# Performance work log

Measured on AMD Instinct MI355X. Metric: run time of the kernel, lower is better.

## Reference

```python
import jax, jax.numpy as jnp
import numpy as np

N, E, G = 10000, 100000, 16
NS, NV = 128, 64            # scalar (0e) / vector (1o) channel counts
DIM = NS + 3 * NV           # 320 flattened feature dim
NSP = 4                     # num_species; edge one-hot has NSP**2 entries
FC_IN = 128                 # edge length embedding size
GATES = NV                  # one gate scalar per gated vector channel
EPS = 1e-5


def _split(x):
    # flattened irreps layout: [NS scalars | NV vectors * 3 components]
    return x[:, :NS], x[:, NS:].reshape(x.shape[0], NV, 3)


def _merge(s, v):
    return jnp.concatenate([s, v.reshape(v.shape[0], -1)], axis=-1)


def setup_inputs() -> dict:
    key = jax.random.key(0)
    ks = jax.random.split(key, 32)
    def nrm(i, shape):
        return jax.random.normal(ks[i], shape, jnp.float32)
    return {
        'node_fea': nrm(0, (N, DIM)),
        'edge_one_hot': jax.random.uniform(ks[1], (E, NSP * NSP), jnp.float32),
        'edge_sh': nrm(2, (E, 4)),
        'edge_fea': nrm(3, (E, DIM)),
        'edge_length_embedded': jax.random.uniform(ks[4], (E, FC_IN), jnp.float32),
        'edge_index': jax.random.randint(ks[5], (2, E), 0, N),
        'batch': jnp.sort(jax.random.randint(ks[6], (N,), 0, G)),
        # self-connection FCTP: edge irreps x species-pair scalars -> out irreps
        'Wsc_s': nrm(7, (NS, NSP * NSP, NS)),
        'Wsc_v': nrm(8, (NV, NSP * NSP, NV)),
        # lin_pre (per-l equivariant linear, bias on scalars only)
        'Wpre0': nrm(9, (NS, NS)), 'bpre0': jnp.zeros((NS,), jnp.float32),
        'Wpre1': nrm(10, (NV, NV)),
        # separate-weight tensor product paths (fea_in x spherical harmonics)
        'Wss': nrm(11, (3 * NS, NS + GATES)),   # 0e x 0e -> 0e
        'Wvs': nrm(12, (3 * NV, NS + GATES)),   # 1o . 1o -> 0e
        'Wsv': nrm(13, (3 * NS, NV)),           # 0e x 1o -> 1o
        'Wvv': nrm(14, (3 * NV, NV)),           # 1o x 0e -> 1o
        # radial MLP (fc): edge_length_embedded -> per-channel conv weights
        'Wf1': nrm(15, (FC_IN, 64)) / np.sqrt(FC_IN), 'bf1': jnp.zeros((64,), jnp.float32),
        'Wf2': nrm(16, (64, 64)) / 8.0, 'bf2': jnp.zeros((64,), jnp.float32),
        'Wf3': nrm(17, (64, NS + NV)) / 8.0, 'bf3': jnp.zeros((NS + NV,), jnp.float32),
        # lin_post
        'Wpost0': nrm(18, (NS, NS)), 'bpost0': jnp.zeros((NS,), jnp.float32),
        'Wpost1': nrm(19, (NV, NV)),
        # e3LayerNorm affine params
        'gamma_s': jnp.ones((NS,), jnp.float32), 'beta_s': jnp.zeros((NS,), jnp.float32),
        'gamma_v': jnp.ones((NV,), jnp.float32),
    }


def reference(node_fea, edge_one_hot, edge_sh, edge_fea, edge_length_embedded,
              edge_index, batch, Wsc_s, Wsc_v, Wpre0, bpre0, Wpre1,
              Wss, Wvs, Wsv, Wvv, Wf1, bf1, Wf2, bf2, Wf3, bf3,
              Wpost0, bpost0, Wpost1, gamma_s, beta_s, gamma_v):
    i, j = edge_index[0], edge_index[1]
    batch_edge = batch[i]
    es, ev = _split(edge_fea)

    # --- self connection: FullyConnectedTensorProduct(edge_fea, one_hot) ---
    sc_s = jnp.einsum('ev,es,vsu->eu', es, edge_one_hot, Wsc_s) / np.sqrt(NS * NSP * NSP)
    sc_v = jnp.einsum('evm,es,vsu->eum', ev, edge_one_hot, Wsc_v) / np.sqrt(NV * NSP * NSP)

    # --- lin_pre on edge features ---
    s = es @ Wpre0 / np.sqrt(NS) + bpre0
    v = jnp.einsum('evm,vu->eum', ev, Wpre1) / np.sqrt(NV)

    # --- gather node features and concat along channel axis ---
    nsf, nvf = _split(node_fea)
    s_in = jnp.concatenate([nsf[i], nsf[j], s], axis=-1)   # [E, 3*NS]
    v_in = jnp.concatenate([nvf[i], nvf[j], v], axis=1)    # [E, 3*NV, 3]

    sh0, sh1 = edge_sh[:, :1], edge_sh[:, 1:4]
    # --- separate-weight tensor product (CG: 1o x 1o -> 0e via dot/sqrt(3)) ---
    out_s = (jnp.einsum('ev,vu->eu', s_in * sh0, Wss) / np.sqrt(3 * NS)
             + jnp.einsum('evm,em,vu->eu', v_in, sh1, Wvs) / np.sqrt(3 * 3 * NV)) / np.sqrt(2.0)
    out_v = (jnp.einsum('ev,em,vu->eum', s_in, sh1, Wsv) / np.sqrt(3 * NS)
             + jnp.einsum('evm,e,vu->eum', v_in, sh0[:, 0], Wvv) / np.sqrt(3 * NV)) / np.sqrt(2.0)

    # --- gate nonlinearity: silu on scalars, sigmoid gates on vectors ---
    z_s = jax.nn.silu(out_s[:, :NS])
    z_v = out_v * jax.nn.sigmoid(out_s[:, NS:])[:, :, None]

    # --- radial MLP -> e3ElementWise per-channel scaling ---
    h = jax.nn.silu(edge_length_embedded @ Wf1 + bf1)
    h = jax.nn.silu(h @ Wf2 + bf2)
    w = h @ Wf3 + bf3                                      # [E, NS+NV]
    z_s = z_s * w[:, :NS]
    z_v = z_v * w[:, NS:, None]

    # --- lin_post ---
    z_s = z_s @ Wpost0 / np.sqrt(NS) + bpost0
    z_v = jnp.einsum('evm,vu->eum', z_v, Wpost1) / np.sqrt(NV)

    # --- add self connection ---
    z_s = z_s + sc_s
    z_v = z_v + sc_v

    # --- e3LayerNorm with per-graph statistics over edges ---
    cnt = jax.ops.segment_sum(jnp.ones((E,), z_s.dtype), batch_edge, num_segments=G)
    cnt = jnp.maximum(cnt, 1.0)
    mean_s = jax.ops.segment_sum(z_s.sum(-1), batch_edge, num_segments=G) / (cnt * NS)
    z_s = z_s - mean_s[batch_edge][:, None]
    var_s = jax.ops.segment_sum((z_s ** 2).sum(-1), batch_edge, num_segments=G) / (cnt * NS)
    z_s = z_s * jax.lax.rsqrt(var_s + EPS)[batch_edge][:, None] * gamma_s + beta_s
    var_v = jax.ops.segment_sum((z_v ** 2).sum((-1, -2)), batch_edge, num_segments=G) / (cnt * NV * 3)
    z_v = z_v * jax.lax.rsqrt(var_v + EPS)[batch_edge][:, None, None] * gamma_v[None, :, None]

    # --- skip connection (same irreps in/out -> plain add) ---
    return edge_fea + _merge(z_s, z_v)
```

## Files before the change

### kernel.cpp

```cpp
#include <hip/hip_runtime.h>
#include <math.h>

typedef unsigned int u32;
typedef unsigned short u16;
typedef __attribute__((ext_vector_type(8))) short bf16x8;
typedef __attribute__((ext_vector_type(4))) float f32x4;

#define E_TOT 100000
constexpr int NS = 128, DIM = 320;

constexpr float SC_S_SCALE = 0.022097086912079608f;
constexpr float SC_V_SCALE = 0.03125f;
constexpr float INV_SQRT128 = 0.08838834764831845f;
constexpr float INV_8 = 0.125f;
constexpr float INV_S384 = 0.05103103630798288f;
constexpr float INV_24 = 0.041666666666666664f;
constexpr float INV_S192 = 0.07216878364870323f;
constexpr float RSQRT2 = 0.7071067811865476f;

#define MFMA __builtin_amdgcn_mfma_f32_16x16x32_bf16
#define F4Z (f32x4){0.f, 0.f, 0.f, 0.f}

__device__ __forceinline__ float sigmoidf_(float x) { return 1.0f / (1.0f + __expf(-x)); }
__device__ __forceinline__ float siluf_(float x) { return x * sigmoidf_(x); }
__device__ __forceinline__ float bf2f(u16 h) {
  u32 u = ((u32)h) << 16;
  return __builtin_bit_cast(float, u);
}
__device__ __forceinline__ u16 f2bf(float f) {
  u32 u = __builtin_bit_cast(u32, f);
  return (u16)((u + 0x7fffu + ((u >> 16) & 1u)) >> 16);
}
__device__ __forceinline__ void gl_lds16(const void* g, void* l) {
  __builtin_amdgcn_global_load_lds((const __attribute__((address_space(1))) u32*)g,
                                   (__attribute__((address_space(3))) u32*)l, 16, 0, 0);
}
__device__ __forceinline__ bf16x8 pack8(float4 r0, float4 r1, float s) {
  bf16x8 a;
  a[0] = (short)f2bf(r0.x * s); a[1] = (short)f2bf(r0.y * s);
  a[2] = (short)f2bf(r0.z * s); a[3] = (short)f2bf(r0.w * s);
  a[4] = (short)f2bf(r1.x * s); a[5] = (short)f2bf(r1.y * s);
  a[6] = (short)f2bf(r1.z * s); a[7] = (short)f2bf(r1.w * s);
  return a;
}
__device__ __forceinline__ void stb(char* base, int row, int rowB, int colByte, u16 v) {
  *(u16*)(base + row * rowB + (colByte ^ ((row & 7) << 4))) = v;
}
__device__ __forceinline__ u16 ldbs(const char* base, int row, int rowB, int colByte) {
  return *(const u16*)(base + row * rowB + (colByte ^ ((row & 7) << 4)));
}
__device__ __forceinline__ bf16x8 ldb8(const char* base, int row, int rowB, int colByte) {
  return *(const bf16x8*)(base + row * rowB + (colByte ^ ((row & 7) << 4)));
}
__device__ __forceinline__ void stb16(char* base, int row, int rowB, int colByte, bf16x8 v) {
  *(bf16x8*)(base + row * rowB + (colByte ^ ((row & 7) << 4))) = v;
}
__device__ __forceinline__ bf16x8 scale8_sh1(bf16x8 v, int m0, float t0, float t1, float t2) {
  float x0 = (m0 == 0) ? t0 : ((m0 == 1) ? t1 : t2);
  float x1 = (m0 == 0) ? t1 : ((m0 == 1) ? t2 : t0);
  float x2 = (m0 == 0) ? t2 : ((m0 == 1) ? t0 : t1);
  bf16x8 r;
  r[0] = (short)f2bf(bf2f((u16)v[0]) * x0); r[1] = (short)f2bf(bf2f((u16)v[1]) * x1);
  r[2] = (short)f2bf(bf2f((u16)v[2]) * x2); r[3] = (short)f2bf(bf2f((u16)v[3]) * x0);
  r[4] = (short)f2bf(bf2f((u16)v[4]) * x1); r[5] = (short)f2bf(bf2f((u16)v[5]) * x2);
  r[6] = (short)f2bf(bf2f((u16)v[6]) * x0); r[7] = (short)f2bf(bf2f((u16)v[7]) * x1);
  return r;
}

#define OW_W2S   0
#define OW_BTV   262144
#define OW_PRE0  327680
#define OW_PRE1X 344064
#define OW_SS    380928
#define OW_VSX   454656
#define OW_SV    565248
#define OW_VVX   589824
#define OW_F1    700416
#define OW_F2    708608
#define OW_F3    712704
#define OW_P0    724992
#define OW_P1X   741376
#define OW_END   778240

__device__ __forceinline__ void frag_uc(int oo, int K, int& up, int& c) {
  int per = (K >> 5) << 9;
  int nt = oo / per, r = oo % per;
  int kc = r >> 9, r2 = r & 511;
  int ln = r2 >> 3, j = r2 & 7;
  up = nt * 16 + (ln & 15);
  c = kc * 32 + (ln >> 4) * 8 + j;
}

__global__ __launch_bounds__(256) void k_prep(
    const float* __restrict__ Wsc_s, const float* __restrict__ Wsc_v,
    const float* __restrict__ Wpre0, const float* __restrict__ Wpre1,
    const float* __restrict__ Wss, const float* __restrict__ Wvs,
    const float* __restrict__ Wsv, const float* __restrict__ Wvv,
    const float* __restrict__ Wf1, const float* __restrict__ Wf2,
    const float* __restrict__ Wf3, const float* __restrict__ Wpost0,
    const float* __restrict__ Wpost1, u16* __restrict__ dst) {
  int o = blockIdx.x * 256 + threadIdx.x;
  if (o >= OW_END) return;
  float v;
  int up, c;
  if (o < OW_BTV) {
    int u = o >> 11, k = o & 2047, s = k >> 7, vv = k & 127;
    v = Wsc_s[((size_t)(vv * 16 + s)) * 128 + u];
  } else if (o < OW_PRE0) {
    int oo = o - OW_BTV; int u = oo >> 10, k = oo & 1023, s = k >> 6, vv = k & 63;
    v = Wsc_v[((size_t)(vv * 16 + s)) * 64 + u];
  } else if (o < OW_PRE1X) {
    frag_uc(o - OW_PRE0, 128, up, c);
    v = Wpre0[c * 128 + up] * INV_SQRT128;
  } else if (o < OW_SS) {
    frag_uc(o - OW_PRE1X, 192, up, c);
    int u = up / 3, m = up % 3, vv = c / 3, mp = c % 3;
    v = (m == mp) ? Wpre1[vv * 64 + u] * INV_8 : 0.f;
  } else if (o < OW_VSX) {
    frag_uc(o - OW_SS, 384, up, c);
    v = Wss[c * 192 + up] * (INV_S384 * RSQRT2);
  } else if (o < OW_SV) {
    frag_uc(o - OW_VSX, 576, up, c);
    int p = c / 192, r = c % 192, K = p * 64 + r / 3;
    v = Wvs[K * 192 + up] * (INV_24 * RSQRT2);
  } else if (o < OW_VVX) {
    frag_uc(o - OW_SV, 384, up, c);
    v = Wsv[c * 64 + up] * (INV_S384 * RSQRT2);
  } else if (o < OW_F1) {
    frag_uc(o - OW_VVX, 576, up, c);
    int u = up / 3, m = up % 3, p = c / 192, r = c % 192, vv = r / 3, mp = r % 3;
    v = (m == mp) ? Wvv[(p * 64 + vv) * 64 + u] * (INV_S192 * RSQRT2) : 0.f;
  } else if (o < OW_F2) {
    frag_uc(o - OW_F1, 128, up, c);
    v = Wf1[c * 64 + up];
  } else if (o < OW_F3) {
    frag_uc(o - OW_F2, 64, up, c);
    v = Wf2[c * 64 + up];
  } else if (o < OW_P0) {
    frag_uc(o - OW_F3, 64, up, c);
    v = Wf3[c * 192 + up];
  } else if (o < OW_P1X) {
    frag_uc(o - OW_P0, 128, up, c);
    v = Wpost0[c * 128 + up] * INV_SQRT128;
  } else {
    frag_uc(o - OW_P1X, 192, up, c);
    int u = up / 3, m = up % 3, vv = c / 3, mp = c % 3;
    v = (m == mp) ? Wpost1[vv * 64 + u] * INV_8 : 0.f;
  }
  dst[o] = f2bf(v);
}

#define MEs 64
__global__ __launch_bounds__(256, 2) void k_sc_s(
    const float* __restrict__ edge_fea, const float* __restrict__ ohp,
    const u16* __restrict__ W2s, float* __restrict__ out) {
  __shared__ u16 esB[64][136];
  __shared__ float ohL[64][16];
  __shared__ u16 Abuf[64 * 128];
  __shared__ u16 Bbuf[128 * 128];
  const int t = threadIdx.x;
  const int lane = t & 63, ww = t >> 6;
  const int e0 = blockIdx.x * MEs;
  const int nE = min(MEs, E_TOT - e0);

  for (int o = t; o < 64 * 32; o += 256) {
    int e = o >> 5, c4 = (o & 31) << 2;
    float4 x = (e < nE) ? *(const float4*)&edge_fea[(size_t)(e0 + e) * DIM + c4]
                        : make_float4(0.f, 0.f, 0.f, 0.f);
    esB[e][c4 + 0] = f2bf(x.x); esB[e][c4 + 1] = f2bf(x.y);
    esB[e][c4 + 2] = f2bf(x.z); esB[e][c4 + 3] = f2bf(x.w);
  }
  for (int o = t; o < 64 * 16; o += 256) {
    int e = o >> 4, s = o & 15;
    ohL[e][s] = (e < nE) ? ohp[(size_t)(e0 + e) * 16 + s] : 0.f;
  }
  __syncthreads();

  f32x4 acc[4][2];
  #pragma unroll
  for (int a = 0; a < 4; ++a)
    #pragma unroll
    for (int b = 0; b < 2; ++b) acc[a][b] = F4Z;

  for (int s = 0; s < 16; ++s) {
    {
      const char* sb = (const char*)W2s + s * 256;
      #pragma unroll
      for (int it = 0; it < 8; ++it) {
        int n = it * 256 + t;
        int u = n >> 4, gp = n & 15, g = gp ^ (u & 7);
        gl_lds16(sb + (size_t)u * 4096 + g * 16, (char*)Bbuf + n * 16);
      }
    }
    #pragma unroll
    for (int it = 0; it < 4; ++it) {
      int n = it * 256 + t;
      int e = n >> 4, gp = n & 15, g = gp ^ (e & 7);
      float ohs = ohL[e][s];
      union { uint4 q; u16 h[8]; } in, ov;
      in.q = *(const uint4*)&esB[e][g * 8];
      #pragma unroll
      for (int j = 0; j < 8; ++j) ov.h[j] = f2bf(bf2f(in.h[j]) * ohs);
      *(uint4*)((char*)Abuf + e * 256 + gp * 16) = ov.q;
    }
    __syncthreads();

    const int cbl = (lane >> 4) << 4;
    #pragma unroll
    for (int ks = 0; ks < 4; ++ks) {
      int cbyte = ks * 64 + cbl;
      bf16x8 bfr[2], afr[4];
      #pragma unroll
      for (int ct = 0; ct < 2; ++ct) {
        int u = ww * 32 + ct * 16 + (lane & 15);
        bfr[ct] = *(const bf16x8*)((const char*)Bbuf + u * 256 + (cbyte ^ ((u & 7) << 4)));
      }
      #pragma unroll
      for (int rt = 0; rt < 4; ++rt) {
        int e = rt * 16 + (lane & 15);
        afr[rt] = *(const bf16x8*)((const char*)Abuf + e * 256 + (cbyte ^ ((e & 7) << 4)));
      }
      #pragma unroll
      for (int rt = 0; rt < 4; ++rt)
        #pragma unroll
        for (int ct = 0; ct < 2; ++ct)
          acc[rt][ct] = MFMA(afr[rt], bfr[ct], acc[rt][ct], 0, 0, 0);
    }
    __syncthreads();
  }

  #pragma unroll
  for (int rt = 0; rt < 4; ++rt) {
    int ebase = rt * 16 + ((lane >> 4) << 2);
    #pragma unroll
    for (int ct = 0; ct < 2; ++ct) {
      int u = ww * 32 + ct * 16 + (lane & 15);
      #pragma unroll
      for (int j = 0; j < 4; ++j) {
        int ee = ebase + j;
        if (ee < nE) out[(size_t)(e0 + ee) * DIM + u] = acc[rt][ct][j] * SC_S_SCALE;
      }
    }
  }
}

__global__ __launch_bounds__(256, 2) void k_sc_v(
    const float* __restrict__ edge_fea, const float* __restrict__ ohp,
    const u16* __restrict__ Btv, float* __restrict__ out) {
  __shared__ u16 evT[3][64][72];
  __shared__ float ohL[64][16];
  __shared__ u16 Abuf[192 * 64];
  __shared__ u16 Bbuf[64 * 64];
  const int t = threadIdx.x;
  const int lane = t & 63, ww = t >> 6;
  const int e0 = blockIdx.x * MEs;
  const int nE = min(MEs, E_TOT - e0);

  for (int o = t; o < 64 * 192; o += 256) {
    int e = o / 192, c = o % 192;
    int v = c / 3, m = c % 3;
    float x = (e < nE) ? edge_fea[(size_t)(e0 + e) * DIM + NS + c] : 0.f;
    evT[m][e][v] = f2bf(x);
  }
  for (int o = t; o < 64 * 16; o += 256) {
    int e = o >> 4, s = o & 15;
    ohL[e][s] = (e < nE) ? ohp[(size_t)(e0 + e) * 16 + s] : 0.f;
  }
  __syncthreads();

  f32x4 acc[12];
  #pragma unroll
  for (int a = 0; a < 12; ++a) acc[a] = F4Z;

  for (int s = 0; s < 16; ++s) {
    #pragma unroll
    for (int it = 0; it < 2; ++it) {
      int n = it * 256 + t;
      int u = n >> 3, gp = n & 7, g = gp ^ (u & 7);
      gl_lds16((const char*)Btv + (size_t)u * 2048 + s * 128 + g * 16, (char*)Bbuf + n * 16);
    }
    #pragma unroll
    for (int it = 0; it < 6; ++it) {
      int n = it * 256 + t;
      int r = n >> 3, gp = n & 7, g = gp ^ (r & 7);
      int e = r / 3, m = r - e * 3;
      float ohs = ohL[e][s];
      union { uint4 q; u16 h[8]; } in, ov;
      in.q = *(const uint4*)&evT[m][e][g * 8];
      #pragma unroll
      for (int j = 0; j < 8; ++j) ov.h[j] = f2bf(bf2f(in.h[j]) * ohs);
      *(uint4*)((char*)Abuf + r * 128 + gp * 16) = ov.q;
    }
    __syncthreads();

    const int cbl = (lane >> 4) << 4;
    #pragma unroll
    for (int ks = 0; ks < 2; ++ks) {
      int cbyte = ks * 64 + cbl;
      int u = ww * 16 + (lane & 15);
      bf16x8 bfr = *(const bf16x8*)((const char*)Bbuf + u * 128 + (cbyte ^ ((u & 7) << 4)));
      #pragma unroll
      for (int rt = 0; rt < 12; ++rt) {
        int r = rt * 16 + (lane & 15);
        bf16x8 afr = *(const bf16x8*)((const char*)Abuf + r * 128 + (cbyte ^ ((r & 7) << 4)));
        acc[rt] = MFMA(afr, bfr, acc[rt], 0, 0, 0);
      }
    }
    __syncthreads();
  }

  #pragma unroll
  for (int rt = 0; rt < 12; ++rt) {
    int rbase = rt * 16 + ((lane >> 4) << 2);
    int u = ww * 16 + (lane & 15);
    #pragma unroll
    for (int j = 0; j < 4; ++j) {
      int r = rbase + j;
      int e = r / 3, m = r - e * 3;
      if (e < nE) out[(size_t)(e0 + e) * DIM + NS + u * 3 + m] = acc[rt][j] * SC_V_SCALE;
    }
  }
}

#define A_SZ 78592
__global__ __launch_bounds__(512, 4) void k_chain(
    const float* __restrict__ node_fea, const float* __restrict__ edge_sh,
    const float* __restrict__ edge_fea, const float* __restrict__ elen,
    const int* __restrict__ eidx, const u16* __restrict__ wbf,
    const float* __restrict__ bpre0, const float* __restrict__ bf1,
    const float* __restrict__ bf2, const float* __restrict__ bf3,
    const float* __restrict__ bpost0, float* __restrict__ out) {
  __shared__ char AR[A_SZ];
  float* shF = (float*)(AR + 77824);
  int* ijL = (int*)(AR + 78336);
  const int t = threadIdx.x, lane = t & 63, wv = t >> 6;
  const int l15 = lane & 15, q8 = lane >> 4, q4 = q8 << 2, cbl = q8 << 4;
  const int e0 = blockIdx.x * 32;

#define SA(b) (AR + (b) * 8192)
#define VA(b) (AR + 24576 + (b) * 12288)
  char* wB = AR;
  char* zsB = AR + 12288;
  char* gateB = AR + 20480;
  char* zvB = AR + 24576;
  char* t1B = AR + 61440;
  char* hB = AR + 65536;
  char* elB = AR + 69632;

  if (t < 64) { int p = t >> 5, e = t & 31; ijL[p * 32 + e] = eidx[p * E_TOT + e0 + e]; }
  if (t >= 64 && t < 192) { int o = t - 64; shF[o] = edge_sh[(size_t)e0 * 4 + o]; }
  __syncthreads();

  for (int o = t; o < 1280; o += 512) {
    int c = o % 40, e = o / 40;
    const float* src = edge_fea + (size_t)(e0 + e) * 320 + c * 8;
    float4 r0 = *(const float4*)src, r1 = *(const float4*)(src + 4);
    bf16x8 v = pack8(r0, r1, 1.f);
    if (c < 16) stb16(SA(2), e, 256, c * 16, v);
    else        stb16(VA(2), e, 384, (c - 16) * 16, v);
  }
  for (int o = t; o < 2560; o += 512) {
    int c = o % 40, tmp = o / 40, e = tmp & 31, p = tmp >> 5;
    const float* src = node_fea + (size_t)ijL[p * 32 + e] * 320 + c * 8;
    float4 r0 = *(const float4*)src, r1 = *(const float4*)(src + 4);
    bf16x8 v = pack8(r0, r1, 1.f);
    if (c < 16) stb16(SA(p), e, 256, c * 16, v);
    else        stb16(VA(p), e, 384, (c - 16) * 16, v);
  }
  for (int o = t; o < 512; o += 512) {
    int c = o & 15, e = o >> 4;
    const float* src = elen + (size_t)(e0 + e) * 128 + c * 8;
    float4 r0 = *(const float4*)src, r1 = *(const float4*)(src + 4);
    stb16(elB, e, 256, c * 16, pack8(r0, r1, 1.f));
  }
  __syncthreads();

  f32x4 acc[8];
  #pragma unroll
  for (int a = 0; a < 8; ++a) acc[a] = F4Z;
  if (wv < 4) {
    for (int kc = 0; kc < 6; ++kc) {
      bf16x8 a0 = ldb8(VA(2), l15, 384, kc * 64 + cbl);
      bf16x8 a1 = ldb8(VA(2), 16 + l15, 384, kc * 64 + cbl);
      #pragma unroll
      for (int i = 0; i < 3; ++i) {
        int nt = wv * 3 + i;
        bf16x8 b = *(const bf16x8*)(wbf + OW_PRE1X + (((size_t)nt * 6 + kc) << 9) + lane * 8);
        acc[i] = MFMA(a0, b, acc[i], 0, 0, 0);
        acc[3 + i] = MFMA(a1, b, acc[3 + i], 0, 0, 0);
      }
    }
  } else if (wv < 6) {
    for (int kc = 0; kc < 4; ++kc) {
      bf16x8 a0 = ldb8(SA(2), l15, 256, kc * 64 + cbl);
      bf16x8 a1 = ldb8(SA(2), 16 + l15, 256, kc * 64 + cbl);
      #pragma unroll
      for (int i = 0; i < 4; ++i) {
        int nt = (wv - 4) * 4 + i;
        bf16x8 b = *(const bf16x8*)(wbf + OW_PRE0 + (((size_t)nt * 4 + kc) << 9) + lane * 8);
        acc[i] = MFMA(a0, b, acc[i], 0, 0, 0);
        acc[4 + i] = MFMA(a1, b, acc[4 + i], 0, 0, 0);
      }
    }
  } else {
    for (int kc = 0; kc < 4; ++kc) {
      bf16x8 a0 = ldb8(elB, l15, 256, kc * 64 + cbl);
      bf16x8 a1 = ldb8(elB, 16 + l15, 256, kc * 64 + cbl);
      #pragma unroll
      for (int i = 0; i < 2; ++i) {
        int nt = (wv - 6) * 2 + i;
        bf16x8 b = *(const bf16x8*)(wbf + OW_F1 + (((size_t)nt * 4 + kc) << 9) + lane * 8);
        acc[i] = MFMA(a0, b, acc[i], 0, 0, 0);
        acc[2 + i] = MFMA(a1, b, acc[2 + i], 0, 0, 0);
      }
    }
  }
  __syncthreads();
  if (wv < 4) {
    #pragma unroll
    for (int mt = 0; mt < 2; ++mt)
      #pragma unroll
      for (int i = 0; i < 3; ++i) {
        int up = (wv * 3 + i) * 16 + l15;
        #pragma unroll
        for (int j = 0; j < 4; ++j)
          stb(VA(2), mt * 16 + q4 + j, 384, up * 2, f2bf(acc[mt * 3 + i][j]));
      }
  } else if (wv < 6) {
    #pragma unroll
    for (int i = 0; i < 4; ++i) {
      int u = ((wv - 4) * 4 + i) * 16 + l15;
      float bias = bpre0[u];
      #pragma unroll
      for (int mt = 0; mt < 2; ++mt)
        #pragma unroll
        for (int j = 0; j < 4; ++j)
          stb(SA(2), mt * 16 + q4 + j, 256, u * 2, f2bf(acc[mt * 4 + i][j] + bias));
    }
  } else {
    #pragma unroll
    for (int i = 0; i < 2; ++i) {
      int u = ((wv - 6) * 2 + i) * 16 + l15;
      float bias = bf1[u];
      #pragma unroll
      for (int mt = 0; mt < 2; ++mt)
        #pragma unroll
        for (int j = 0; j < 4; ++j)
          stb(hB, mt * 16 + q4 + j, 128, u * 2, f2bf(siluf_(acc[mt * 2 + i][j] + bias)));
    }
  }
  __syncthreads();

  f32x4 os[4] = {F4Z, F4Z, F4Z, F4Z};
  f32x4 h2a = F4Z;
  {
    const int hmt = wv >> 2, hnt = wv & 3;
    #pragma unroll
    for (int kc = 0; kc < 2; ++kc) {
      bf16x8 a = ldb8(hB, hmt * 16 + l15, 128, kc * 64 + cbl);
      bf16x8 b = *(const bf16x8*)(wbf + OW_F2 + (((size_t)hnt * 2 + kc) << 9) + lane * 8);
      h2a = MFMA(a, b, h2a, 0, 0, 0);
    }
  }
  if (wv < 6) {
    for (int kc = 0; kc < 12; ++kc) {
      int buf = kc >> 2, cB = (kc & 3) * 64 + cbl;
      bf16x8 a0 = ldb8(SA(buf), l15, 256, cB);
      bf16x8 a1 = ldb8(SA(buf), 16 + l15, 256, cB);
      #pragma unroll
      for (int i = 0; i < 2; ++i) {
        int nt = wv * 2 + i;
        bf16x8 b = *(const bf16x8*)(wbf + OW_SS + (((size_t)nt * 12 + kc) << 9) + lane * 8);
        os[i] = MFMA(a0, b, os[i], 0, 0, 0);
        os[2 + i] = MFMA(a1, b, os[2 + i], 0, 0, 0);
      }
    }
    #pragma unroll
    for (int mt = 0; mt < 2; ++mt)
      #pragma unroll
      for (int i = 0; i < 2; ++i)
        #pragma unroll
        for (int j = 0; j < 4; ++j)
          os[mt * 2 + i][j] *= shF[(mt * 16 + q4 + j) * 4 + 0];
    float sa0 = shF[l15 * 4 + 1], sa1 = shF[l15 * 4 + 2], sa2 = shF[l15 * 4 + 3];
    float sb0 = shF[(16 + l15) * 4 + 1], sb1 = shF[(16 + l15) * 4 + 2], sb2 = shF[(16 + l15) * 4 + 3];
    for (int p = 0; p < 3; ++p)
      for (int kc6 = 0; kc6 < 6; ++kc6) {
        int cB = kc6 * 64 + cbl;
        int m0 = (2 * (kc6 + q8)) % 3;
        bf16x8 a0 = scale8_sh1(ldb8(VA(p), l15, 384, cB), m0, sa0, sa1, sa2);
        bf16x8 a1 = scale8_sh1(ldb8(VA(p), 16 + l15, 384, cB), m0, sb0, sb1, sb2);
        int kcg = p * 6 + kc6;
        #pragma unroll
        for (int i = 0; i < 2; ++i) {
          int nt = wv * 2 + i;
          bf16x8 b = *(const bf16x8*)(wbf + OW_VSX + (((size_t)nt * 18 + kcg) << 9) + lane * 8);
          os[i] = MFMA(a0, b, os[i], 0, 0, 0);
          os[2 + i] = MFMA(a1, b, os[2 + i], 0, 0, 0);
        }
      }
  } else {
    for (int kc = 0; kc < 12; ++kc) {
      int buf = kc >> 2, cB = (kc & 3) * 64 + cbl;
      bf16x8 a0 = ldb8(SA(buf), l15, 256, cB);
      bf16x8 a1 = ldb8(SA(buf), 16 + l15, 256, cB);
      #pragma unroll
      for (int i = 0; i < 2; ++i) {
        int nt = (wv - 6) * 2 + i;
        bf16x8 b = *(const bf16x8*)(wbf + OW_SV + (((size_t)nt * 12 + kc) << 9) + lane * 8);
        os[i] = MFMA(a0, b, os[i], 0, 0, 0);
        os[2 + i] = MFMA(a1, b, os[2 + i], 0, 0, 0);
      }
    }
  }
  __syncthreads();
  {
    const int hmt = wv >> 2;
    int u = (wv & 3) * 16 + l15;
    float bias = bf2[u];
    #pragma unroll
    for (int j = 0; j < 4; ++j)
      stb(hB, hmt * 16 + q4 + j, 128, u * 2, f2bf(siluf_(h2a[j] + bias)));
  }
  if (wv >= 6) {
    #pragma unroll
    for (int mt = 0; mt < 2; ++mt)
      #pragma unroll
      for (int i = 0; i < 2; ++i) {
        int u = ((wv - 6) * 2 + i) * 16 + l15;
        #pragma unroll
        for (int j = 0; j < 4; ++j)
          stb(t1B, mt * 16 + q4 + j, 128, u * 2, f2bf(os[mt * 2 + i][j]));
      }
  }
  __syncthreads();

  {
    f32x4 wa[3] = {F4Z, F4Z, F4Z};
    const int mtw = wv >> 2;
    #pragma unroll
    for (int kc = 0; kc < 2; ++kc) {
      bf16x8 a = ldb8(hB, mtw * 16 + l15, 128, kc * 64 + cbl);
      #pragma unroll
      for (int i = 0; i < 3; ++i) {
        int nt = (wv & 3) * 3 + i;
        bf16x8 b = *(const bf16x8*)(wbf + OW_F3 + (((size_t)nt * 2 + kc) << 9) + lane * 8);
        wa[i] = MFMA(a, b, wa[i], 0, 0, 0);
      }
    }
    #pragma unroll
    for (int i = 0; i < 3; ++i) {
      int up = ((wv & 3) * 3 + i) * 16 + l15;
      float bias = bf3[up];
      #pragma unroll
      for (int j = 0; j < 4; ++j)
        stb(wB, mtw * 16 + q4 + j, 384, up * 2, f2bf(wa[i][j] + bias));
    }
  }
  __syncthreads();

  if (wv < 6) {
    #pragma unroll
    for (int mt = 0; mt < 2; ++mt)
      #pragma unroll
      for (int i = 0; i < 2; ++i) {
        int up = (wv * 2 + i) * 16 + l15;
        #pragma unroll
        for (int j = 0; j < 4; ++j) {
          int e = mt * 16 + q4 + j;
          float w_ = bf2f(ldbs(wB, e, 384, up * 2));
          float o_ = os[mt * 2 + i][j];
          if (up < 128) stb(zsB, e, 256, up * 2, f2bf(siluf_(o_) * w_));
          else stb(gateB, e, 128, (up - 128) * 2, f2bf(sigmoidf_(o_) * w_));
        }
      }
  }
  f32x4 ov[3] = {F4Z, F4Z, F4Z};
  {
    const int mtv = wv >> 2;
    for (int p = 0; p < 3; ++p)
      for (int kc6 = 0; kc6 < 6; ++kc6) {
        int cB = kc6 * 64 + cbl;
        bf16x8 a = ldb8(VA(p), mtv * 16 + l15, 384, cB);
        int kcg = p * 6 + kc6;
        #pragma unroll
        for (int i = 0; i < 3; ++i) {
          int nt = (wv & 3) * 3 + i;
          bf16x8 b = *(const bf16x8*)(wbf + OW_VVX + (((size_t)nt * 18 + kcg) << 9) + lane * 8);
          ov[i] = MFMA(a, b, ov[i], 0, 0, 0);
        }
      }
  }
  __syncthreads();
  {
    const int mtv = wv >> 2;
    #pragma unroll
    for (int i = 0; i < 3; ++i) {
      int up = ((wv & 3) * 3 + i) * 16 + l15;
      int u = (up * 683) >> 11, m = up - 3 * u;
      #pragma unroll
      for (int j = 0; j < 4; ++j) {
        int e = mtv * 16 + q4 + j;
        float t1v = bf2f(ldbs(t1B, e, 128, u * 2));
        float g = bf2f(ldbs(gateB, e, 128, u * 2));
        float val = ov[i][j] * shF[e * 4 + 0] + t1v * shF[e * 4 + 1 + m];
        stb(zvB, e, 384, up * 2, f2bf(val * g));
      }
    }
  }
  __syncthreads();

  {
    f32x4 p0[2] = {F4Z, F4Z};
    #pragma unroll
    for (int kc = 0; kc < 4; ++kc) {
      int cB = kc * 64 + cbl;
      bf16x8 a0 = ldb8(zsB, l15, 256, cB);
      bf16x8 a1 = ldb8(zsB, 16 + l15, 256, cB);
      bf16x8 b = *(const bf16x8*)(wbf + OW_P0 + (((size_t)wv * 4 + kc) << 9) + lane * 8);
      p0[0] = MFMA(a0, b, p0[0], 0, 0, 0);
      p0[1] = MFMA(a1, b, p0[1], 0, 0, 0);
    }
    int u = wv * 16 + l15;
    float bias = bpost0[u];
    #pragma unroll
    for (int mt = 0; mt < 2; ++mt)
      #pragma unroll
      for (int j = 0; j < 4; ++j) {
        size_t o = (size_t)(e0 + mt * 16 + q4 + j) * DIM + u;
        out[o] = out[o] + p0[mt][j] + bias;
      }
  }
  {
    f32x4 p1[3] = {F4Z, F4Z, F4Z};
    const int mtv = wv >> 2;
    #pragma unroll
    for (int kc = 0; kc < 6; ++kc) {
      int cB = kc * 64 + cbl;
      bf16x8 a = ldb8(zvB, mtv * 16 + l15, 384, cB);
      #pragma unroll
      for (int i = 0; i < 3; ++i) {
        int nt = (wv & 3) * 3 + i;
        bf16x8 b = *(const bf16x8*)(wbf + OW_P1X + (((size_t)nt * 6 + kc) << 9) + lane * 8);
        p1[i] = MFMA(a, b, p1[i], 0, 0, 0);
      }
    }
    #pragma unroll
    for (int i = 0; i < 3; ++i) {
      int up = ((wv & 3) * 3 + i) * 16 + l15;
      #pragma unroll
      for (int j = 0; j < 4; ++j) {
        size_t o = (size_t)(e0 + mtv * 16 + q4 + j) * DIM + 128 + up;
        out[o] = out[o] + p1[i][j];
      }
    }
  }
#undef SA
#undef VA
}

__global__ __launch_bounds__(256) void k_stats(
    const float* __restrict__ out, const int* __restrict__ eidx,
    const int* __restrict__ batch, float* __restrict__ stats) {
  __shared__ float gacc[16][4];
  const int t = threadIdx.x;
  if (t < 64) ((float*)gacc)[t] = 0.0f;
  __syncthreads();
  const int el = t >> 4, l = t & 15;
  for (int ebase = blockIdx.x * 16; ebase < E_TOT; ebase += gridDim.x * 16) {
    int e = ebase + el;
    const float* z = out + (size_t)e * DIM;
    float s1 = 0, s2 = 0, s2v = 0;
    for (int c = l; c < 128; c += 16) { float x = z[c]; s1 += x; s2 += x * x; }
    for (int c = 128 + l; c < DIM; c += 16) { float x = z[c]; s2v += x * x; }
    #pragma unroll
    for (int msk = 8; msk; msk >>= 1) {
      s1 += __shfl_xor(s1, msk);
      s2 += __shfl_xor(s2, msk);
      s2v += __shfl_xor(s2v, msk);
    }
    if (l == 0) {
      int g = batch[eidx[e]];
      atomicAdd(&gacc[g][0], 1.0f);
      atomicAdd(&gacc[g][1], s1);
      atomicAdd(&gacc[g][2], s2);
      atomicAdd(&gacc[g][3], s2v);
    }
  }
  __syncthreads();
  if (t < 64) {
    float v = gacc[t >> 2][t & 3];
    if (v != 0.0f) atomicAdd(&stats[(t >> 2) * 16 + (t & 3)], v);
  }
}

__global__ __launch_bounds__(256) void k_norm(
    const float* __restrict__ edge_fea, const int* __restrict__ eidx,
    const int* __restrict__ batch, const float* __restrict__ stats,
    const float* __restrict__ gamma_s, const float* __restrict__ beta_s,
    const float* __restrict__ gamma_v, float* __restrict__ out) {
  __shared__ float meanL[16], invsL[16], invvL[16];
  __shared__ int gL[16];
  const int t = threadIdx.x;
  const int e0 = blockIdx.x * 16;
  if (t < 16) {
    float cnt = fmaxf(stats[t * 16 + 0], 1.0f);
    float m = stats[t * 16 + 1] / (cnt * 128.0f);
    float var = stats[t * 16 + 2] / (cnt * 128.0f) - m * m;
    meanL[t] = m;
    invsL[t] = rsqrtf(var + 1e-5f);
    invvL[t] = rsqrtf(stats[t * 16 + 3] / (cnt * 192.0f) + 1e-5f);
  }
  if (t >= 32 && t < 48) gL[t - 32] = batch[eidx[e0 + t - 32]];
  __syncthreads();
  for (int o = t; o < 16 * 80; o += 256) {
    int e = o / 80, q = o % 80;
    size_t idx = (size_t)(e0 + e) * 80 + q;
    float4 z = ((const float4*)out)[idx];
    float4 ef = ((const float4*)edge_fea)[idx];
    int g = gL[e];
    float4 r;
    if (q < 32) {
      int c = q * 4;
      r.x = (z.x - meanL[g]) * invsL[g] * gamma_s[c + 0] + beta_s[c + 0] + ef.x;
      r.y = (z.y - meanL[g]) * invsL[g] * gamma_s[c + 1] + beta_s[c + 1] + ef.y;
      r.z = (z.z - meanL[g]) * invsL[g] * gamma_s[c + 2] + beta_s[c + 2] + ef.z;
      r.w = (z.w - meanL[g]) * invsL[g] * gamma_s[c + 3] + beta_s[c + 3] + ef.w;
    } else {
      int cc = q * 4 - 128;
      r.x = z.x * invvL[g] * gamma_v[(cc + 0) / 3] + ef.x;
      r.y = z.y * invvL[g] * gamma_v[(cc + 1) / 3] + ef.y;
      r.z = z.z * invvL[g] * gamma_v[(cc + 2) / 3] + ef.z;
      r.w = z.w * invvL[g] * gamma_v[(cc + 3) / 3] + ef.w;
    }
    ((float4*)out)[idx] = r;
  }
}

extern "C" void kernel_launch(void* const* d_in, const int* in_sizes, int n_in,
                              void* d_out, int out_size, void* d_ws, size_t ws_size,
                              hipStream_t stream) {
  const float* node_fea = (const float*)d_in[0];
  const float* edge_oh  = (const float*)d_in[1];
  const float* edge_sh  = (const float*)d_in[2];
  const float* edge_fea = (const float*)d_in[3];
  const float* elen     = (const float*)d_in[4];
  const int*   eidx     = (const int*)d_in[5];
  const int*   batch    = (const int*)d_in[6];
  const float* Wsc_s    = (const float*)d_in[7];
  const float* Wsc_v    = (const float*)d_in[8];
  const float* Wpre0    = (const float*)d_in[9];
  const float* bpre0    = (const float*)d_in[10];
  const float* Wpre1    = (const float*)d_in[11];
  const float* Wss      = (const float*)d_in[12];
  const float* Wvs      = (const float*)d_in[13];
  const float* Wsv      = (const float*)d_in[14];
  const float* Wvv      = (const float*)d_in[15];
  const float* Wf1      = (const float*)d_in[16];
  const float* bf1      = (const float*)d_in[17];
  const float* Wf2      = (const float*)d_in[18];
  const float* bf2      = (const float*)d_in[19];
  const float* Wf3      = (const float*)d_in[20];
  const float* bf3      = (const float*)d_in[21];
  const float* Wpost0   = (const float*)d_in[22];
  const float* bpost0   = (const float*)d_in[23];
  const float* Wpost1   = (const float*)d_in[24];
  const float* gamma_s  = (const float*)d_in[25];
  const float* beta_s   = (const float*)d_in[26];
  const float* gamma_v  = (const float*)d_in[27];
  float* out = (float*)d_out;

  char* ws = (char*)d_ws;
  float* stats = (float*)ws;
  u16* wbf = (u16*)(ws + 1024);

  hipMemsetAsync(stats, 0, 16 * 16 * sizeof(float), stream);
  k_prep<<<(OW_END + 255) / 256, 256, 0, stream>>>(
      Wsc_s, Wsc_v, Wpre0, Wpre1, Wss, Wvs, Wsv, Wvv,
      Wf1, Wf2, Wf3, Wpost0, Wpost1, wbf);
  const int nblk64 = (E_TOT + MEs - 1) / MEs;
  k_sc_s<<<nblk64, 256, 0, stream>>>(edge_fea, edge_oh, wbf + OW_W2S, out);
  k_sc_v<<<nblk64, 256, 0, stream>>>(edge_fea, edge_oh, wbf + OW_BTV, out);
  k_chain<<<E_TOT / 32, 512, 0, stream>>>(node_fea, edge_sh, edge_fea, elen, eidx,
                                          wbf, bpre0, bf1, bf2, bf3, bpost0, out);
  k_stats<<<512, 256, 0, stream>>>(out, eidx, batch, stats);
  k_norm<<<E_TOT / 16, 256, 0, stream>>>(edge_fea, eidx, batch, stats,
                                         gamma_s, beta_s, gamma_v, out);
}
```

Measured before the change: 760.1 us.

## Fuse self-connection kernels and apply one-hot scaling after MFMA

Merges the scalar and vector self-connection kernels into one launch that reads each edge_fea row once. Instead of rebuilding a one-hot-scaled A tile in LDS for every species pair, it keeps the A fragments fixed (registers for scalars, LDS for vectors), computes the plain product per species pair, and scales the partial result by the one-hot weight in fp32 registers. The output scale constants are folded into the bf16 weights during prep. k_stats is vectorised to use float4 loads. This removes per-iteration A-tile construction and one kernel launch, in exchange for more register pressure and extra fp32 multiply-adds per species pair.

```diff
diff --git a/kernel.cpp b/kernel.cpp
--- a/kernel.cpp
+++ b/kernel.cpp
@@ -105,10 +105,10 @@
   int up, c;
   if (o < OW_BTV) {
     int u = o >> 11, k = o & 2047, s = k >> 7, vv = k & 127;
-    v = Wsc_s[((size_t)(vv * 16 + s)) * 128 + u];
+    v = Wsc_s[((size_t)(vv * 16 + s)) * 128 + u] * SC_S_SCALE;
   } else if (o < OW_PRE0) {
     int oo = o - OW_BTV; int u = oo >> 10, k = oo & 1023, s = k >> 6, vv = k & 63;
-    v = Wsc_v[((size_t)(vv * 16 + s)) * 64 + u];
+    v = Wsc_v[((size_t)(vv * 16 + s)) * 64 + u] * SC_V_SCALE;
   } else if (o < OW_PRE1X) {
     frag_uc(o - OW_PRE0, 128, up, c);
     v = Wpre0[c * 128 + up] * INV_SQRT128;
@@ -151,174 +151,139 @@
 }
 
 #define MEs 64
-__global__ __launch_bounds__(256, 2) void k_sc_s(
+__global__ __launch_bounds__(256, 2) void k_sc(
     const float* __restrict__ edge_fea, const float* __restrict__ ohp,
-    const u16* __restrict__ W2s, float* __restrict__ out) {
-  __shared__ u16 esB[64][136];
+    const u16* __restrict__ W2s, const u16* __restrict__ Btv,
+    float* __restrict__ out) {
+  __shared__ char esB[16384];
+  __shared__ char evT[24576];
   __shared__ float ohL[64][16];
-  __shared__ u16 Abuf[64 * 128];
-  __shared__ u16 Bbuf[128 * 128];
-  const int t = threadIdx.x;
-  const int lane = t & 63, ww = t >> 6;
+  __shared__ char Bbuf[32768];
+  const int t = threadIdx.x, lane = t & 63, ww = t >> 6;
+  const int l15 = lane & 15, q8 = lane >> 4, q4 = q8 << 2, cbl = q8 << 4;
   const int e0 = blockIdx.x * MEs;
   const int nE = min(MEs, E_TOT - e0);
 
-  for (int o = t; o < 64 * 32; o += 256) {
-    int e = o >> 5, c4 = (o & 31) << 2;
-    float4 x = (e < nE) ? *(const float4*)&edge_fea[(size_t)(e0 + e) * DIM + c4]
-                        : make_float4(0.f, 0.f, 0.f, 0.f);
-    esB[e][c4 + 0] = f2bf(x.x); esB[e][c4 + 1] = f2bf(x.y);
-    esB[e][c4 + 2] = f2bf(x.z); esB[e][c4 + 3] = f2bf(x.w);
-  }
-  for (int o = t; o < 64 * 16; o += 256) {
+  for (int o = t; o < 2560; o += 256) {
+    int c = o % 40, e = o / 40;
+    float4 r0 = make_float4(0.f, 0.f, 0.f, 0.f), r1 = r0;
+    if (e < nE) {
+      const float* src = edge_fea + (size_t)(e0 + e) * 320 + c * 8;
+      r0 = *(const float4*)src; r1 = *(const float4*)(src + 4);
+    }
+    if (c < 16) stb16(esB, e, 256, c * 16, pack8(r0, r1, 1.f));
+    else {
+      int base = (c - 16) * 8;
+      float vals[8] = {r0.x, r0.y, r0.z, r0.w, r1.x, r1.y, r1.z, r1.w};
+      #pragma unroll
+      for (int z = 0; z < 8; ++z) {
+        int cc = base + z;
+        stb(evT, 3 * e + cc % 3, 128, (cc / 3) * 2, f2bf(vals[z]));
+      }
+    }
+  }
+  for (int o = t; o < 1024; o += 256) {
     int e = o >> 4, s = o & 15;
     ohL[e][s] = (e < nE) ? ohp[(size_t)(e0 + e) * 16 + s] : 0.f;
   }
   __syncthreads();
 
-  f32x4 acc[4][2];
-  #pragma unroll
-  for (int a = 0; a < 4; ++a)
-    #pragma unroll
-    for (int b = 0; b < 2; ++b) acc[a][b] = F4Z;
-
-  for (int s = 0; s < 16; ++s) {
-    {
+  {
+    bf16x8 afh[4][4];
+    #pragma unroll
+    for (int rt = 0; rt < 4; ++rt)
+      #pragma unroll
+      for (int ks = 0; ks < 4; ++ks)
+        afh[rt][ks] = ldb8(esB, rt * 16 + l15, 256, ks * 64 + cbl);
+    f32x4 acc[8];
+    #pragma unroll
+    for (int i = 0; i < 8; ++i) acc[i] = F4Z;
+    for (int s = 0; s < 16; ++s) {
       const char* sb = (const char*)W2s + s * 256;
       #pragma unroll
       for (int it = 0; it < 8; ++it) {
         int n = it * 256 + t;
         int u = n >> 4, gp = n & 15, g = gp ^ (u & 7);
-        gl_lds16(sb + (size_t)u * 4096 + g * 16, (char*)Bbuf + n * 16);
-      }
-    }
-    #pragma unroll
-    for (int it = 0; it < 4; ++it) {
-      int n = it * 256 + t;
-      int e = n >> 4, gp = n & 15, g = gp ^ (e & 7);
-      float ohs = ohL[e][s];
-      union { uint4 q; u16 h[8]; } in, ov;
-      in.q = *(const uint4*)&esB[e][g * 8];
-      #pragma unroll
-      for (int j = 0; j < 8; ++j) ov.h[j] = f2bf(bf2f(in.h[j]) * ohs);
-      *(uint4*)((char*)Abuf + e * 256 + gp * 16) = ov.q;
-    }
-    __syncthreads();
-
-    const int cbl = (lane >> 4) << 4;
-    #pragma unroll
-    for (int ks = 0; ks < 4; ++ks) {
-      int cbyte = ks * 64 + cbl;
-      bf16x8 bfr[2], afr[4];
+        gl_lds16(sb + (size_t)u * 4096 + g * 16, Bbuf + n * 16);
+      }
+      __syncthreads();
+      f32x4 tmp[8];
+      #pragma unroll
+      for (int i = 0; i < 8; ++i) tmp[i] = F4Z;
+      #pragma unroll
+      for (int ks = 0; ks < 4; ++ks) {
+        bf16x8 b0 = ldb8(Bbuf, ww * 32 + l15, 256, ks * 64 + cbl);
+        bf16x8 b1 = ldb8(Bbuf, ww * 32 + 16 + l15, 256, ks * 64 + cbl);
+        #pragma unroll
+        for (int rt = 0; rt < 4; ++rt) {
+          tmp[rt * 2 + 0] = MFMA(afh[rt][ks], b0, tmp[rt * 2 + 0], 0, 0, 0);
+          tmp[rt * 2 + 1] = MFMA(afh[rt][ks], b1, tmp[rt * 2 + 1], 0, 0, 0);
+        }
+      }
+      #pragma unroll
+      for (int rt = 0; rt < 4; ++rt)
+        #pragma unroll
+        for (int j = 0; j < 4; ++j) {
+          float oh = ohL[rt * 16 + q4 + j][s];
+          acc[rt * 2 + 0][j] += oh * tmp[rt * 2 + 0][j];
+          acc[rt * 2 + 1][j] += oh * tmp[rt * 2 + 1][j];
+        }
+      __syncthreads();
+    }
+    #pragma unroll
+    for (int rt = 0; rt < 4; ++rt)
       #pragma unroll
       for (int ct = 0; ct < 2; ++ct) {
-        int u = ww * 32 + ct * 16 + (lane & 15);
-        bfr[ct] = *(const bf16x8*)((const char*)Bbuf + u * 256 + (cbyte ^ ((u & 7) << 4)));
-      }
-      #pragma unroll
-      for (int rt = 0; rt < 4; ++rt) {
-        int e = rt * 16 + (lane & 15);
-        afr[rt] = *(const bf16x8*)((const char*)Abuf + e * 256 + (cbyte ^ ((e & 7) << 4)));
-      }
-      #pragma unroll
-      for (int rt = 0; rt < 4; ++rt)
-        #pragma unroll
-        for (int ct = 0; ct < 2; ++ct)
-          acc[rt][ct] = MFMA(afr[rt], bfr[ct], acc[rt][ct], 0, 0, 0);
-    }
-    __syncthreads();
-  }
-
-  #pragma unroll
-  for (int rt = 0; rt < 4; ++rt) {
-    int ebase = rt * 16 + ((lane >> 4) << 2);
-    #pragma unroll
-    for (int ct = 0; ct < 2; ++ct) {
-      int u = ww * 32 + ct * 16 + (lane & 15);
+        int u = ww * 32 + ct * 16 + l15;
+        #pragma unroll
+        for (int j = 0; j < 4; ++j) {
+          int e = rt * 16 + q4 + j;
+          if (e < nE) out[(size_t)(e0 + e) * DIM + u] = acc[rt * 2 + ct][j];
+        }
+      }
+  }
+
+  {
+    f32x4 acc[12];
+    #pragma unroll
+    for (int i = 0; i < 12; ++i) acc[i] = F4Z;
+    for (int s = 0; s < 16; ++s) {
+      #pragma unroll
+      for (int it = 0; it < 2; ++it) {
+        int n = it * 256 + t;
+        int u = n >> 3, gp = n & 7, g = gp ^ (u & 7);
+        gl_lds16((const char*)Btv + (size_t)u * 2048 + s * 128 + g * 16, Bbuf + n * 16);
+      }
+      __syncthreads();
+      f32x4 tmp[12];
+      #pragma unroll
+      for (int i = 0; i < 12; ++i) tmp[i] = F4Z;
+      #pragma unroll
+      for (int ks = 0; ks < 2; ++ks) {
+        bf16x8 b = ldb8(Bbuf, ww * 16 + l15, 128, ks * 64 + cbl);
+        #pragma unroll
+        for (int rt = 0; rt < 12; ++rt) {
+          bf16x8 a = ldb8(evT, rt * 16 + l15, 128, ks * 64 + cbl);
+          tmp[rt] = MFMA(a, b, tmp[rt], 0, 0, 0);
+        }
+      }
+      #pragma unroll
+      for (int rt = 0; rt < 12; ++rt)
+        #pragma unroll
+        for (int j = 0; j < 4; ++j) {
+          int r = rt * 16 + q4 + j;
+          acc[rt][j] += ohL[r / 3][s] * tmp[rt][j];
+        }
+      __syncthreads();
+    }
+    int u = ww * 16 + l15;
+    #pragma unroll
+    for (int rt = 0; rt < 12; ++rt)
       #pragma unroll
       for (int j = 0; j < 4; ++j) {
-        int ee = ebase + j;
-        if (ee < nE) out[(size_t)(e0 + ee) * DIM + u] = acc[rt][ct][j] * SC_S_SCALE;
-      }
-    }
-  }
-}
-
-__global__ __launch_bounds__(256, 2) void k_sc_v(
-    const float* __restrict__ edge_fea, const float* __restrict__ ohp,
-    const u16* __restrict__ Btv, float* __restrict__ out) {
-  __shared__ u16 evT[3][64][72];
-  __shared__ float ohL[64][16];
-  __shared__ u16 Abuf[192 * 64];
-  __shared__ u16 Bbuf[64 * 64];
-  const int t = threadIdx.x;
-  const int lane = t & 63, ww = t >> 6;
-  const int e0 = blockIdx.x * MEs;
-  const int nE = min(MEs, E_TOT - e0);
-
-  for (int o = t; o < 64 * 192; o += 256) {
-    int e = o / 192, c = o % 192;
-    int v = c / 3, m = c % 3;
-    float x = (e < nE) ? edge_fea[(size_t)(e0 + e) * DIM + NS + c] : 0.f;
-    evT[m][e][v] = f2bf(x);
-  }
-  for (int o = t; o < 64 * 16; o += 256) {
-    int e = o >> 4, s = o & 15;
-    ohL[e][s] = (e < nE) ? ohp[(size_t)(e0 + e) * 16 + s] : 0.f;
-  }
-  __syncthreads();
-
-  f32x4 acc[12];
-  #pragma unroll
-  for (int a = 0; a < 12; ++a) acc[a] = F4Z;
-
-  for (int s = 0; s < 16; ++s) {
-    #pragma unroll
-    for (int it = 0; it < 2; ++it) {
-      int n = it * 256 + t;
-      int u = n >> 3, gp = n & 7, g = gp ^ (u & 7);
-      gl_lds16((const char*)Btv + (size_t)u * 2048 + s * 128 + g * 16, (char*)Bbuf + n * 16);
-    }
-    #pragma unroll
-    for (int it = 0; it < 6; ++it) {
-      int n = it * 256 + t;
-      int r = n >> 3, gp = n & 7, g = gp ^ (r & 7);
-      int e = r / 3, m = r - e * 3;
-      float ohs = ohL[e][s];
-      union { uint4 q; u16 h[8]; } in, ov;
-      in.q = *(const uint4*)&evT[m][e][g * 8];
-      #pragma unroll
-      for (int j = 0; j < 8; ++j) ov.h[j] = f2bf(bf2f(in.h[j]) * ohs);
-      *(uint4*)((char*)Abuf + r * 128 + gp * 16) = ov.q;
-    }
-    __syncthreads();
-
-    const int cbl = (lane >> 4) << 4;
-    #pragma unroll
-    for (int ks = 0; ks < 2; ++ks) {
-      int cbyte = ks * 64 + cbl;
-      int u = ww * 16 + (lane & 15);
-      bf16x8 bfr = *(const bf16x8*)((const char*)Bbuf + u * 128 + (cbyte ^ ((u & 7) << 4)));
-      #pragma unroll
-      for (int rt = 0; rt < 12; ++rt) {
-        int r = rt * 16 + (lane & 15);
-        bf16x8 afr = *(const bf16x8*)((const char*)Abuf + r * 128 + (cbyte ^ ((r & 7) << 4)));
-        acc[rt] = MFMA(afr, bfr, acc[rt], 0, 0, 0);
-      }
-    }
-    __syncthreads();
-  }
-
-  #pragma unroll
-  for (int rt = 0; rt < 12; ++rt) {
-    int rbase = rt * 16 + ((lane >> 4) << 2);
-    int u = ww * 16 + (lane & 15);
-    #pragma unroll
-    for (int j = 0; j < 4; ++j) {
-      int r = rbase + j;
-      int e = r / 3, m = r - e * 3;
-      if (e < nE) out[(size_t)(e0 + e) * DIM + NS + u * 3 + m] = acc[rt][j] * SC_V_SCALE;
-    }
+        int r = rt * 16 + q4 + j, e = r / 3, m = r - e * 3;
+        if (e < nE) out[(size_t)(e0 + e) * DIM + 128 + u * 3 + m] = acc[rt][j];
+      }
   }
 }
 
@@ -669,10 +634,17 @@
   const int el = t >> 4, l = t & 15;
   for (int ebase = blockIdx.x * 16; ebase < E_TOT; ebase += gridDim.x * 16) {
     int e = ebase + el;
-    const float* z = out + (size_t)e * DIM;
+    const float4* z4 = (const float4*)(out + (size_t)e * DIM);
     float s1 = 0, s2 = 0, s2v = 0;
-    for (int c = l; c < 128; c += 16) { float x = z[c]; s1 += x; s2 += x * x; }
-    for (int c = 128 + l; c < DIM; c += 16) { float x = z[c]; s2v += x * x; }
+    float4 a = z4[l], b = z4[16 + l];
+    s1 = a.x + a.y + a.z + a.w + b.x + b.y + b.z + b.w;
+    s2 = a.x * a.x + a.y * a.y + a.z * a.z + a.w * a.w +
+         b.x * b.x + b.y * b.y + b.z * b.z + b.w * b.w;
+    #pragma unroll
+    for (int p = 0; p < 3; ++p) {
+      float4 c = z4[32 + p * 16 + l];
+      s2v += c.x * c.x + c.y * c.y + c.z * c.z + c.w * c.w;
+    }
     #pragma unroll
     for (int msk = 8; msk; msk >>= 1) {
       s1 += __shfl_xor(s1, msk);
@@ -779,8 +751,7 @@
       Wsc_s, Wsc_v, Wpre0, Wpre1, Wss, Wvs, Wsv, Wvv,
       Wf1, Wf2, Wf3, Wpost0, Wpost1, wbf);
   const int nblk64 = (E_TOT + MEs - 1) / MEs;
-  k_sc_s<<<nblk64, 256, 0, stream>>>(edge_fea, edge_oh, wbf + OW_W2S, out);
-  k_sc_v<<<nblk64, 256, 0, stream>>>(edge_fea, edge_oh, wbf + OW_BTV, out);
+  k_sc<<<nblk64, 256, 0, stream>>>(edge_fea, edge_oh, wbf + OW_W2S, wbf + OW_BTV, out);
   k_chain<<<E_TOT / 32, 512, 0, stream>>>(node_fea, edge_sh, edge_fea, elen, eidx,
                                           wbf, bpre0, bf1, bf2, bf3, bpost0, out);
   k_stats<<<512, 256, 0, stream>>>(out, eidx, batch, stats);
```

New measurement: 659.2 us. 13.3% less time.
